# Kernel optimization log

Hardware: AMD Instinct MI355X
Metric: run time of the kernel (lower is better)

Reference implementation:

```python
import jax, jax.numpy as jnp
import numpy as np
from jax import lax

NPOINT, RADIUS, NSAMPLE = 1024, 0.2, 32
EPS = 1e-5

def _fps(xyz, npoint):
    # farthest point sampling, xyz [B,N,3] -> idx [B,npoint]
    B, N, _ = xyz.shape
    def body(carry, _):
        dist, far = carry  # [B,N], [B]
        c = jnp.take_along_axis(xyz, far[:, None, None], axis=1)  # [B,1,3]
        d = jnp.sum((xyz - c) ** 2, -1)
        dist = jnp.minimum(dist, d)
        nxt = jnp.argmax(dist, -1).astype(jnp.int32)
        return (dist, nxt), far
    init = (jnp.full((B, N), 1e10, xyz.dtype), jnp.zeros((B,), jnp.int32))
    _, idx = lax.scan(body, init, None, length=npoint)
    return jnp.transpose(idx)  # [B,npoint]

def _index_points(pts, idx):
    # pts [B,N,C], idx [B,...] int -> [B,...,C]
    return jax.vmap(lambda p, i: p[i])(pts, idx)

def _ball_query(radius, nsample, xyz, new_xyz):
    B, N, _ = xyz.shape
    sqr = (jnp.sum(new_xyz ** 2, -1)[:, :, None] + jnp.sum(xyz ** 2, -1)[:, None, :]
           - 2.0 * jnp.einsum('bsc,bnc->bsn', new_xyz, xyz))  # [B,S,N]
    base = jnp.arange(N, dtype=jnp.int32)[None, None, :]
    idx = jnp.where(sqr > radius ** 2, N, base)
    idx = jnp.sort(idx, -1)[..., :nsample]  # [B,S,K]
    first = idx[..., :1]
    return jnp.where(idx == N, jnp.broadcast_to(first, idx.shape), idx)

def _mlp_bn_relu(x, w, b, g, beta):
    # x [B,C,K,S]; 1x1 conv == channel GEMM; BN uses batch stats (training mode)
    x = jnp.einsum('bcks,oc->boks', x, w) + b[None, :, None, None]
    mu = jnp.mean(x, axis=(0, 2, 3), keepdims=True)
    var = jnp.var(x, axis=(0, 2, 3), keepdims=True)
    x = (x - mu) * lax.rsqrt(var + EPS) * g[None, :, None, None] + beta[None, :, None, None]
    return jax.nn.relu(x)

def setup_inputs() -> dict:
    key = jax.random.key(0)
    ks = jax.random.split(key, 16)
    B, N, D = 16, 4096, 3
    mlp = [64, 64, 128]
    inp = {
        'xyz': jax.random.uniform(ks[0], (B, 3, N), jnp.float32),
        'features': jax.random.normal(ks[1], (B, D, N), jnp.float32),
    }
    last = 3 + D
    for i, c in enumerate(mlp):
        inp[f'w{i}'] = jax.random.normal(ks[2 + 4 * i], (c, last), jnp.float32) * (1.0 / np.sqrt(last))
        inp[f'b{i}'] = jnp.zeros((c,), jnp.float32)
        inp[f'g{i}'] = jnp.ones((c,), jnp.float32)
        inp[f'bt{i}'] = jnp.zeros((c,), jnp.float32)
        last = c
    return inp

def reference(xyz, features, w0, b0, g0, bt0, w1, b1, g1, bt1, w2, b2, g2, bt2):
    xyz_t = jnp.transpose(xyz, (0, 2, 1))        # [B,N,3]
    feat_t = jnp.transpose(features, (0, 2, 1))  # [B,N,D]
    fps_idx = _fps(xyz_t, NPOINT)
    new_xyz = _index_points(xyz_t, fps_idx)      # [B,S,3]
    idx = _ball_query(RADIUS, NSAMPLE, xyz_t, new_xyz)  # [B,S,K]
    grouped_xyz = _index_points(xyz_t, idx) - new_xyz[:, :, None, :]  # [B,S,K,3]
    grouped_feat = _index_points(feat_t, idx)                          # [B,S,K,D]
    x = jnp.concatenate([grouped_xyz, grouped_feat], -1)               # [B,S,K,3+D]
    x = jnp.transpose(x, (0, 3, 2, 1))           # [B,C,K,S]
    for (w, b, g, beta) in ((w0, b0, g0, bt0), (w1, b1, g1, bt1), (w2, b2, g2, bt2)):
        x = _mlp_bn_relu(x, w, b, g, beta)
    new_features = jnp.max(x, axis=2)            # [B,C',S]
    return jnp.transpose(new_xyz, (0, 2, 1)), new_features
```

## Files before the change

kernel.cpp:

```cpp
#include <hip/hip_runtime.h>
#include <hip/hip_bf16.h>
#include <stdint.h>

#define NB 16
#define NPTS 4096
#define NS 1024
#define NK 32
#define NT_COLS (NB*NS*NK)
#define NBUCK 64

typedef __hip_bfloat16 bf16;
typedef __attribute__((ext_vector_type(8))) short short8;
typedef __attribute__((ext_vector_type(4))) float floatx4;
typedef __attribute__((ext_vector_type(2))) float f32x2;

__device__ __forceinline__ unsigned short f2bf_bits(float v) {
  bf16 b = __float2bfloat16(v);
  return *(unsigned short*)&b;
}

template<int CTRL, int RM, int BM>
__device__ __forceinline__ float fmax_dpp(float x) {
  int o = __builtin_amdgcn_update_dpp(__float_as_int(x), __float_as_int(x),
                                      CTRL, RM, BM, false);
  return fmaxf(x, __int_as_float(o));
}
template<int CTRL, int RM>
__device__ __forceinline__ float add_dpp(float x) {
  int o = __builtin_amdgcn_update_dpp(0, __float_as_int(x), CTRL, RM, 0xF, true);
  return __fadd_rn(x, __int_as_float(o));
}
__device__ __forceinline__ float add16_dpp(float x) {
  x = add_dpp<0x111,0xF>(x); x = add_dpp<0x112,0xF>(x);
  x = add_dpp<0x114,0xF>(x); x = add_dpp<0x118,0xF>(x);
  return x;
}
__device__ __forceinline__ float add64_dpp(float x) {
  x = add_dpp<0x111,0xF>(x); x = add_dpp<0x112,0xF>(x);
  x = add_dpp<0x114,0xF>(x); x = add_dpp<0x118,0xF>(x);
  x = add_dpp<0x142,0xA>(x);
  x = add_dpp<0x143,0xC>(x);
  return x;
}

__global__ __launch_bounds__(256) void k_fps(const float* __restrict__ xyz,
                                             float* __restrict__ newxyz,
                                             float* __restrict__ out0,
                                             float* __restrict__ zero_region) {
  const int b = blockIdx.x;
  const int t = threadIdx.x;
  {
    float* zp = zero_region + (size_t)b*2048 + t;
    #pragma unroll
    for (int j = 0; j < 8; ++j) zp[j*256] = 0.f;
  }
  __shared__ float xs[NPTS], ys[NPTS], zs[NPTS];
  __shared__ float selx[NS], sely[NS], selz[NS];
  __shared__ float2 pair[2][4];
  const float* p = xyz + (size_t)b * 3 * NPTS;
  for (int i = t; i < NPTS; i += 256) {
    xs[i] = p[i];
    ys[i] = p[NPTS + i];
    zs[i] = p[2*NPTS + i];
  }
  __syncthreads();
  f32x2 px[8], py[8], pz[8];
  float dist[16];
  const int p0 = t * 16;
  #pragma unroll
  for (int j2 = 0; j2 < 8; ++j2) {
    px[j2] = (f32x2){xs[p0+2*j2], xs[p0+2*j2+1]};
    py[j2] = (f32x2){ys[p0+2*j2], ys[p0+2*j2+1]};
    pz[j2] = (f32x2){zs[p0+2*j2], zs[p0+2*j2+1]};
    dist[2*j2] = 1e10f; dist[2*j2+1] = 1e10f;
  }
  const int lane = t & 63, wv = t >> 6;
  int cur = 0;
  for (int i = 0; i < NS; ++i) {
    float cx = xs[cur], cy = ys[cur], cz = zs[cur];
    if (t == 0) { selx[i] = cx; sely[i] = cy; selz[i] = cz; }
    if (i == NS-1) break;
    const f32x2 ncx = (f32x2){-cx, -cx};
    const f32x2 ncy = (f32x2){-cy, -cy};
    const f32x2 ncz = (f32x2){-cz, -cz};
    float bv = -1.0f; int bi = p0;
    #pragma unroll
    for (int j2 = 0; j2 < 8; ++j2) {
      f32x2 d;
      {
        #pragma clang fp contract(off)
        f32x2 dx = px[j2] + ncx;
        f32x2 dy = py[j2] + ncy;
        f32x2 dz = pz[j2] + ncz;
        d = dx*dx + dy*dy + dz*dz;
      }
      float nd0 = fminf(dist[2*j2],   d.x);
      float nd1 = fminf(dist[2*j2+1], d.y);
      dist[2*j2] = nd0; dist[2*j2+1] = nd1;
      if (nd0 > bv) { bv = nd0; bi = p0 + 2*j2; }
      if (nd1 > bv) { bv = nd1; bi = p0 + 2*j2 + 1; }
    }
    float x = bv;
    x = fmax_dpp<0x111,0xF,0xF>(x);
    x = fmax_dpp<0x112,0xF,0xF>(x);
    x = fmax_dpp<0x114,0xF,0xF>(x);
    x = fmax_dpp<0x118,0xF,0xF>(x);
    x = fmax_dpp<0x142,0xA,0xF>(x);
    x = fmax_dpp<0x143,0xC,0xF>(x);
    float M = __int_as_float(__builtin_amdgcn_readlane(__float_as_int(x), 63));
    unsigned long long mk = __ballot(bv == M);
    int sl  = (int)__builtin_ctzll(mk);
    int wbi = __builtin_amdgcn_readlane(bi, sl);
    if ((t & 63) == 0) pair[i & 1][wv] = make_float2(M, __int_as_float(wbi));
    __syncthreads();
    const float4* pb = (const float4*)&pair[i & 1][0];
    float4 q01 = pb[0], q23 = pb[1];
    float bestv = q01.x; int besti = __float_as_int(q01.y);
    if (q01.z > bestv) { bestv = q01.z; besti = __float_as_int(q01.w); }
    if (q23.x > bestv) { bestv = q23.x; besti = __float_as_int(q23.y); }
    if (q23.z > bestv) { bestv = q23.z; besti = __float_as_int(q23.w); }
    cur = besti;
  }
  __syncthreads();
  for (int i = t; i < NS; i += 256) {
    float vx = selx[i], vy = sely[i], vz = selz[i];
    size_t q = (size_t)b*3*NS + i;
    out0[q] = vx; out0[q + NS] = vy; out0[q + 2*NS] = vz;
    size_t o = (size_t)(b*NS + i)*3;
    newxyz[o] = vx; newxyz[o+1] = vy; newxyz[o+2] = vz;
  }
}

__global__ __launch_bounds__(256) void k_ballq(const float* __restrict__ xyz,
                                               const float* __restrict__ newxyz,
                                               int* __restrict__ idx) {
  __shared__ float xs[NPTS], ys[NPTS], zs[NPTS];
  const int b  = blockIdx.x >> 8;
  const int s  = (blockIdx.x & 255) * 4 + (threadIdx.x >> 6);
  const int lane = threadIdx.x & 63;
  const float* p = xyz + (size_t)b * 3 * NPTS;
  for (int i = threadIdx.x; i < NPTS; i += 256) {
    xs[i] = p[i];
    ys[i] = p[NPTS + i];
    zs[i] = p[2*NPTS + i];
  }
  __syncthreads();
  const size_t nq = (size_t)(b*NS + s)*3;
  const float nx = newxyz[nq], ny = newxyz[nq+1], nz = newxyz[nq+2];
  const float sn = __fadd_rn(__fadd_rn(__fmul_rn(nx,nx), __fmul_rn(ny,ny)), __fmul_rn(nz,nz));
  const float R2 = (float)(0.2*0.2);
  int* out = idx + (size_t)(b*NS + s) * NK;
  int cnt = 0, first = 0;
  for (int c0 = 0; c0 < NPTS; c0 += 64) {
    int n = c0 + lane;
    float x = xs[n], y = ys[n], z = zs[n];
    float sx = __fadd_rn(__fadd_rn(__fmul_rn(x,x), __fmul_rn(y,y)), __fmul_rn(z,z));
    float dt = __fadd_rn(__fadd_rn(__fmul_rn(nx,x), __fmul_rn(ny,y)), __fmul_rn(nz,z));
    float sqr = __fsub_rn(__fadd_rn(sn, sx), __fmul_rn(2.0f, dt));
    bool inr = (sqr <= R2);
    unsigned long long m = __ballot(inr);
    if (m != 0ull) {
      if (cnt == 0) first = c0 + (int)__builtin_ctzll(m);
      int rank = __popcll(m & ((1ull << lane) - 1ull));
      int pos = cnt + rank;
      if (inr && pos < NK) out[pos] = n;
      cnt += __popcll(m);
      if (cnt >= NK) break;
    }
  }
  int tot = cnt < NK ? cnt : NK;
  if (lane >= tot && lane < NK) out[lane] = first;
}

__global__ __launch_bounds__(256) void k_moments(const float* __restrict__ xyz,
                                                 const float* __restrict__ feat,
                                                 const float* __restrict__ newxyz,
                                                 const int* __restrict__ idx,
                                                 float* __restrict__ accum) {
  const int t = threadIdx.x;
  float S[6] = {0,0,0,0,0,0};
  float Mm[21];
  #pragma unroll
  for (int k = 0; k < 21; ++k) Mm[k] = 0.f;
  for (int it = 0; it < 8; ++it) {
    const int col = blockIdx.x*2048 + it*256 + t;
    const int bs = col >> 5;
    const int b  = bs >> 10;
    const int n  = idx[col];
    const float* xb = xyz  + (size_t)b*3*NPTS;
    const float* fb = feat + (size_t)b*3*NPTS;
    float u[6];
    u[0] = __fsub_rn(xb[n],        newxyz[(size_t)bs*3]);
    u[1] = __fsub_rn(xb[NPTS+n],   newxyz[(size_t)bs*3+1]);
    u[2] = __fsub_rn(xb[2*NPTS+n], newxyz[(size_t)bs*3+2]);
    u[3] = fb[n];
    u[4] = fb[NPTS+n];
    u[5] = fb[2*NPTS+n];
    int k = 0;
    #pragma unroll
    for (int i = 0; i < 6; ++i) {
      S[i] += u[i];
      #pragma unroll
      for (int j = i; j < 6; ++j) { Mm[k] = fmaf(u[i], u[j], Mm[k]); ++k; }
    }
  }
  const int lane = t & 63;
  float* dst = accum + (size_t)(blockIdx.x & (NBUCK-1))*32;
  #pragma unroll
  for (int i = 0; i < 6; ++i) {
    float s = add64_dpp(S[i]);
    if (lane == 63) atomicAdd(&dst[i], s);
  }
  #pragma unroll
  for (int k = 0; k < 21; ++k) {
    float m = add64_dpp(Mm[k]);
    if (lane == 63) atomicAdd(&dst[6+k], m);
  }
}

__global__ void k_finalize1(const float* __restrict__ accum,
                            const float* __restrict__ w0, const float* __restrict__ b0,
                            const float* __restrict__ g, const float* __restrict__ beta,
                            float* __restrict__ scsh) {
  __shared__ float Sm[27];
  const int t = threadIdx.x;
  if (t < 27) {
    float s = 0.f;
    for (int bkt = 0; bkt < NBUCK; ++bkt) s += accum[(size_t)bkt*32 + t];
    Sm[t] = s;
  }
  __syncthreads();
  if (t < 64) {
    const float* w = w0 + t*6;
    const float b = b0[t];
    float ws = 0.f;
    #pragma unroll
    for (int i = 0; i < 6; ++i) ws = fmaf(w[i], Sm[i], ws);
    float quad = 0.f;
    int k = 6;
    #pragma unroll
    for (int i = 0; i < 6; ++i) {
      #pragma unroll
      for (int j = i; j < 6; ++j) {
        float c = w[i]*w[j];
        if (j > i) c *= 2.f;
        quad = fmaf(c, Sm[k], quad);
        ++k;
      }
    }
    const float n = (float)NT_COLS;
    float mean = (ws + n*b) / n;
    float ex2  = (quad + 2.f*b*ws + n*b*b) / n;
    float var  = ex2 - mean*mean;
    if (var < 0.f) var = 0.f;
    float rs = rsqrtf(var + 1e-5f);
    float sc = g[t] * rs;
    scsh[t]    = sc;
    scsh[64+t] = beta[t] - mean * sc;
  }
}

__global__ void k_finalize(const float* __restrict__ accum,
                           const float* __restrict__ g, const float* __restrict__ beta,
                           float* __restrict__ scsh, int C) {
  int o = threadIdx.x;
  if (o < C) {
    float s = 0.f, ss = 0.f;
    for (int bkt = 0; bkt < NBUCK; ++bkt) {
      s  += accum[(size_t)bkt*(2*C) + o];
      ss += accum[(size_t)bkt*(2*C) + C + o];
    }
    const float n = (float)NT_COLS;
    float mu  = s / n;
    float var = ss / n - mu*mu;
    if (var < 0.f) var = 0.f;
    float rs = rsqrtf(var + 1e-5f);
    float sc = g[o] * rs;
    scsh[o]   = sc;
    scsh[C+o] = beta[o] - mu * sc;
  }
}

#define XT_STRIDE 72

__global__ __launch_bounds__(256) void k_layer2_mfma(
    const float* __restrict__ xyz,
    const float* __restrict__ feat,
    const float* __restrict__ newxyz,
    const int*   __restrict__ idx,
    const float* __restrict__ w0g,
    const float* __restrict__ b0g,
    const float* __restrict__ w1,
    const float* __restrict__ b1,
    const float* __restrict__ scsh,
    float*       __restrict__ accum,
    bf16*        __restrict__ x2) {
  __shared__ short xT[256*XT_STRIDE];
  __shared__ float w0s[64*6];
  __shared__ float b0s[64];
  __shared__ float sc_s[64], sh_s[64], bias_s[64];
  const int t = threadIdx.x;
  const int col0 = blockIdx.x * 256;
  for (int i = t; i < 64*6; i += 256) w0s[i] = w0g[i];
  if (t < 64) {
    b0s[t] = b0g[t];
    sc_s[t] = scsh[t]; sh_s[t] = scsh[64+t];
    bias_s[t] = b1[t];
  }
  __syncthreads();
  {
    const int col = col0 + t;
    const int bs = col >> 5;
    const int b  = bs >> 10;
    const int n  = idx[col];
    const float* xb = xyz  + (size_t)b*3*NPTS;
    const float* fb = feat + (size_t)b*3*NPTS;
    float u[6];
    u[0] = __fsub_rn(xb[n],        newxyz[(size_t)bs*3]);
    u[1] = __fsub_rn(xb[NPTS+n],   newxyz[(size_t)bs*3+1]);
    u[2] = __fsub_rn(xb[2*NPTS+n], newxyz[(size_t)bs*3+2]);
    u[3] = fb[n];
    u[4] = fb[NPTS+n];
    u[5] = fb[2*NPTS+n];
    #pragma unroll
    for (int c0 = 0; c0 < 64; c0 += 8) {
      short8 pk;
      #pragma unroll
      for (int j = 0; j < 8; ++j) {
        const int o = c0 + j;
        float v = b0s[o];
        #pragma unroll
        for (int c = 0; c < 6; ++c) v = fmaf(u[c], w0s[o*6+c], v);
        v = fmaxf(fmaf(v, sc_s[o], sh_s[o]), 0.f);
        pk[j] = (short)f2bf_bits(v);
      }
      *((short8*)&xT[t*XT_STRIDE + c0]) = pk;
    }
  }
  __syncthreads();
  const int lane = t & 63, wv = t >> 6;
  const int qd = lane >> 4, ln = lane & 15;
  short8 A[4][2];
  #pragma unroll
  for (int rt = 0; rt < 4; ++rt) {
    #pragma unroll
    for (int kh = 0; kh < 2; ++kh) {
      const float* wp = w1 + (size_t)(rt*16 + ln)*64 + kh*32 + qd*8;
      float4 f0 = *(const float4*)wp;
      float4 f1 = *(const float4*)(wp + 4);
      short8 a;
      a[0]=(short)f2bf_bits(f0.x); a[1]=(short)f2bf_bits(f0.y);
      a[2]=(short)f2bf_bits(f0.z); a[3]=(short)f2bf_bits(f0.w);
      a[4]=(short)f2bf_bits(f1.x); a[5]=(short)f2bf_bits(f1.y);
      a[6]=(short)f2bf_bits(f1.z); a[7]=(short)f2bf_bits(f1.w);
      A[rt][kh] = a;
    }
  }
  floatx4 acc[4][4];
  #pragma unroll
  for (int rt = 0; rt < 4; ++rt)
    #pragma unroll
    for (int ct = 0; ct < 4; ++ct)
      acc[rt][ct] = (floatx4)0.f;
  #pragma unroll
  for (int ct = 0; ct < 4; ++ct) {
    const int coll = wv*64 + ct*16 + ln;
    short8 B0 = *((const short8*)&xT[coll*XT_STRIDE + qd*8]);
    short8 B1 = *((const short8*)&xT[coll*XT_STRIDE + 32 + qd*8]);
    #pragma unroll
    for (int rt = 0; rt < 4; ++rt) {
      acc[rt][ct] = __builtin_amdgcn_mfma_f32_16x16x32_bf16(A[rt][0], B0, acc[rt][ct], 0,0,0);
      acc[rt][ct] = __builtin_amdgcn_mfma_f32_16x16x32_bf16(A[rt][1], B1, acc[rt][ct], 0,0,0);
    }
  }
  float* dst = accum + (size_t)(blockIdx.x & (NBUCK-1))*128;
  #pragma unroll
  for (int rt = 0; rt < 4; ++rt) {
    float s[4]  = {0.f,0.f,0.f,0.f};
    float sq[4] = {0.f,0.f,0.f,0.f};
    #pragma unroll
    for (int ct = 0; ct < 4; ++ct) {
      const int col = col0 + wv*64 + ct*16 + ln;
      #pragma unroll
      for (int r = 0; r < 4; ++r) {
        const int o = rt*16 + qd*4 + r;
        float v = acc[rt][ct][r] + bias_s[o];
        x2[(size_t)o*NT_COLS + col] = __float2bfloat16(v);
        s[r] += v; sq[r] = fmaf(v, v, sq[r]);
      }
    }
    #pragma unroll
    for (int r = 0; r < 4; ++r) {
      float a = add16_dpp(s[r]);
      float q = add16_dpp(sq[r]);
      if (ln == 15) {
        const int o = rt*16 + qd*4 + r;
        atomicAdd(&dst[o], a);
        atomicAdd(&dst[64 + o], q);
      }
    }
  }
}

__global__ __launch_bounds__(256) void k_layer3_mfma(
    const bf16*  __restrict__ xin,
    const float* __restrict__ wN,
    const float* __restrict__ bN,
    const float* __restrict__ scsh,
    float*       __restrict__ accum,
    float*       __restrict__ mx) {
  constexpr int CO = 128, RT = CO/16;
  __shared__ short xT[256*XT_STRIDE];
  __shared__ float sc_s[64], sh_s[64], bias_s[CO];
  const int t = threadIdx.x;
  const int col0 = blockIdx.x * 256;
  if (t < 64) { sc_s[t] = scsh[t]; sh_s[t] = scsh[64+t]; }
  if (t < CO) bias_s[t] = bN[t];
  __syncthreads();
  {
    const int col = col0 + t;
    #pragma unroll
    for (int c0 = 0; c0 < 64; c0 += 8) {
      short8 pk;
      #pragma unroll
      for (int j = 0; j < 8; ++j) {
        float v = __bfloat162float(xin[(size_t)(c0+j)*NT_COLS + col]);
        v = fmaxf(fmaf(v, sc_s[c0+j], sh_s[c0+j]), 0.f);
        pk[j] = (short)f2bf_bits(v);
      }
      *((short8*)&xT[t*XT_STRIDE + c0]) = pk;
    }
  }
  __syncthreads();
  const int lane = t & 63, wv = t >> 6;
  const int qd = lane >> 4, ln = lane & 15;
  short8 A[RT][2];
  #pragma unroll
  for (int rt = 0; rt < RT; ++rt) {
    #pragma unroll
    for (int kh = 0; kh < 2; ++kh) {
      const float* wp = wN + (size_t)(rt*16 + ln)*64 + kh*32 + qd*8;
      float4 f0 = *(const float4*)wp;
      float4 f1 = *(const float4*)(wp + 4);
      short8 a;
      a[0]=(short)f2bf_bits(f0.x); a[1]=(short)f2bf_bits(f0.y);
      a[2]=(short)f2bf_bits(f0.z); a[3]=(short)f2bf_bits(f0.w);
      a[4]=(short)f2bf_bits(f1.x); a[5]=(short)f2bf_bits(f1.y);
      a[6]=(short)f2bf_bits(f1.z); a[7]=(short)f2bf_bits(f1.w);
      A[rt][kh] = a;
    }
  }
  floatx4 acc[RT][4];
  #pragma unroll
  for (int rt = 0; rt < RT; ++rt)
    #pragma unroll
    for (int ct = 0; ct < 4; ++ct)
      acc[rt][ct] = (floatx4)0.f;
  #pragma unroll
  for (int ct = 0; ct < 4; ++ct) {
    const int coll = wv*64 + ct*16 + ln;
    short8 B0 = *((const short8*)&xT[coll*XT_STRIDE + qd*8]);
    short8 B1 = *((const short8*)&xT[coll*XT_STRIDE + 32 + qd*8]);
    #pragma unroll
    for (int rt = 0; rt < RT; ++rt) {
      acc[rt][ct] = __builtin_amdgcn_mfma_f32_16x16x32_bf16(A[rt][0], B0, acc[rt][ct], 0,0,0);
      acc[rt][ct] = __builtin_amdgcn_mfma_f32_16x16x32_bf16(A[rt][1], B1, acc[rt][ct], 0,0,0);
    }
  }
  float* dst = accum + (size_t)(blockIdx.x & (NBUCK-1))*(2*CO);
  const int bs0 = (col0 + wv*64) >> 5;
  #pragma unroll
  for (int rt = 0; rt < RT; ++rt) {
    float s[4]  = {0.f,0.f,0.f,0.f};
    float sq[4] = {0.f,0.f,0.f,0.f};
    float mxv[2][4];
    #pragma unroll
    for (int h = 0; h < 2; ++h)
      #pragma unroll
      for (int r = 0; r < 4; ++r) mxv[h][r] = -3.402823466e38f;
    #pragma unroll
    for (int ct = 0; ct < 4; ++ct) {
      #pragma unroll
      for (int r = 0; r < 4; ++r) {
        const int o = rt*16 + qd*4 + r;
        float v = acc[rt][ct][r] + bias_s[o];
        mxv[ct>>1][r] = fmaxf(mxv[ct>>1][r], v);
        s[r] += v; sq[r] = fmaf(v, v, sq[r]);
      }
    }
    #pragma unroll
    for (int h = 0; h < 2; ++h) {
      #pragma unroll
      for (int r = 0; r < 4; ++r) {
        float m = mxv[h][r];
        m = fmax_dpp<0x111,0xF,0xF>(m);
        m = fmax_dpp<0x112,0xF,0xF>(m);
        m = fmax_dpp<0x114,0xF,0xF>(m);
        m = fmax_dpp<0x118,0xF,0xF>(m);
        if (ln == 15) {
          const int o = rt*16 + qd*4 + r;
          mx[(size_t)o*(NT_COLS/NK) + bs0 + h] = m;
        }
      }
    }
    #pragma unroll
    for (int r = 0; r < 4; ++r) {
      float a = add16_dpp(s[r]);
      float q = add16_dpp(sq[r]);
      if (ln == 15) {
        const int o = rt*16 + qd*4 + r;
        atomicAdd(&dst[o], a);
        atomicAdd(&dst[CO + o], q);
      }
    }
  }
}

__global__ __launch_bounds__(256) void k_bnmax(const float* __restrict__ mx,
                                               const float* __restrict__ scsh,
                                               float* __restrict__ out1) {
  const int blk = blockIdx.x;
  const int o = blk & 127;
  const int b = blk >> 7;
  const float sc = scsh[o], sh = scsh[128+o];
  const int s = threadIdx.x * 4;
  float4 v = *(const float4*)(mx + (size_t)o*(NT_COLS/NK) + b*NS + s);
  float4 r;
  r.x = fmaxf(fmaf(v.x, sc, sh), 0.f);
  r.y = fmaxf(fmaf(v.y, sc, sh), 0.f);
  r.z = fmaxf(fmaf(v.z, sc, sh), 0.f);
  r.w = fmaxf(fmaf(v.w, sc, sh), 0.f);
  *(float4*)(out1 + (size_t)(b*128 + o)*NS + s) = r;
}

extern "C" void kernel_launch(void* const* d_in, const int* in_sizes, int n_in,
                              void* d_out, int out_size, void* d_ws, size_t ws_size,
                              hipStream_t stream) {
  const float* xyz  = (const float*)d_in[0];
  const float* feat = (const float*)d_in[1];
  const float* w0 = (const float*)d_in[2];
  const float* b0 = (const float*)d_in[3];
  const float* g0 = (const float*)d_in[4];
  const float* bt0= (const float*)d_in[5];
  const float* w1 = (const float*)d_in[6];
  const float* b1 = (const float*)d_in[7];
  const float* g1 = (const float*)d_in[8];
  const float* bt1= (const float*)d_in[9];
  const float* w2 = (const float*)d_in[10];
  const float* b2 = (const float*)d_in[11];
  const float* g2 = (const float*)d_in[12];
  const float* bt2= (const float*)d_in[13];

  float* out0 = (float*)d_out;
  float* out1 = out0 + (size_t)NB*3*NS;

  char* ws = (char*)d_ws;
  float* accum  = (float*)(ws + 0);
  float* acc_l1 = accum;
  float* acc_l2 = accum + 8192;
  float* acc_l3 = accum + 16384;
  float* scsh   = (float*)(ws + 131072);
  float* newxyz = (float*)(ws + 133120);
  int*   bidx   = (int*)  (ws + 329728);
  bf16*  x2     = (bf16*) (ws + 2426880);
  float* mx3    = (float*)(ws + 136644608);

  k_fps  <<<NB, 256, 0, stream>>>(xyz, newxyz, out0, accum);
  k_ballq<<<NB*256, 256, 0, stream>>>(xyz, newxyz, bidx);

  k_moments  <<<256, 256, 0, stream>>>(xyz, feat, newxyz, bidx, acc_l1);
  k_finalize1<<<1,    64, 0, stream>>>(acc_l1, w0, b0, g0, bt0, scsh + 0);

  k_layer2_mfma<<<NT_COLS/256, 256, 0, stream>>>(xyz, feat, newxyz, bidx,
                                                 w0, b0, w1, b1, scsh + 0,
                                                 acc_l2, x2);
  k_finalize<<<1, 256, 0, stream>>>(acc_l2, g1, bt1, scsh + 128, 64);

  k_layer3_mfma<<<NT_COLS/256, 256, 0, stream>>>(x2, w2, b2, scsh + 128,
                                                 acc_l3, mx3);
  k_finalize<<<1, 256, 0, stream>>>(acc_l3, g2, bt2, scsh + 256, 128);

  k_bnmax <<<NB*128, 256, 0, stream>>>(mx3, scsh + 256, out1);
}
```

Measured before the change: 816.8 us.

## Carry winner coordinates in FPS reduction and pack four batches per block

```diff
diff --git a/kernel.cpp b/kernel.cpp
--- a/kernel.cpp
+++ b/kernel.cpp
@@ -43,47 +43,56 @@
   return x;
 }
 
-__global__ __launch_bounds__(256) void k_fps(const float* __restrict__ xyz,
-                                             float* __restrict__ newxyz,
-                                             float* __restrict__ out0,
-                                             float* __restrict__ zero_region) {
-  const int b = blockIdx.x;
+__global__ __launch_bounds__(1024) void k_fps(const float* __restrict__ xyz,
+                                              float* __restrict__ newxyz,
+                                              float* __restrict__ out0,
+                                              float* __restrict__ zero_region) {
   const int t = threadIdx.x;
   {
-    float* zp = zero_region + (size_t)b*2048 + t;
-    #pragma unroll
-    for (int j = 0; j < 8; ++j) zp[j*256] = 0.f;
-  }
-  __shared__ float xs[NPTS], ys[NPTS], zs[NPTS];
-  __shared__ float selx[NS], sely[NS], selz[NS];
-  __shared__ float2 pair[2][4];
+    float* zp = zero_region + (size_t)blockIdx.x*8192 + t;
+    #pragma unroll
+    for (int j = 0; j < 8; ++j) zp[j*1024] = 0.f;
+  }
+  const int half = t >> 8;
+  const int tl   = t & 255;
+  const int b    = blockIdx.x*4 + half;
+  const int lane = t & 63;
+  const int wv4  = tl >> 6;
+  __shared__ __align__(16) float4 pair[2][4][4];
   const float* p = xyz + (size_t)b * 3 * NPTS;
-  for (int i = t; i < NPTS; i += 256) {
-    xs[i] = p[i];
-    ys[i] = p[NPTS + i];
-    zs[i] = p[2*NPTS + i];
-  }
-  __syncthreads();
+
   f32x2 px[8], py[8], pz[8];
   float dist[16];
-  const int p0 = t * 16;
-  #pragma unroll
-  for (int j2 = 0; j2 < 8; ++j2) {
-    px[j2] = (f32x2){xs[p0+2*j2], xs[p0+2*j2+1]};
-    py[j2] = (f32x2){ys[p0+2*j2], ys[p0+2*j2+1]};
-    pz[j2] = (f32x2){zs[p0+2*j2], zs[p0+2*j2+1]};
-    dist[2*j2] = 1e10f; dist[2*j2+1] = 1e10f;
-  }
-  const int lane = t & 63, wv = t >> 6;
-  int cur = 0;
+  const int p0 = tl * 16;
+  {
+    const float4* xp = (const float4*)(p + p0);
+    const float4* yp = (const float4*)(p + NPTS + p0);
+    const float4* zp4 = (const float4*)(p + 2*NPTS + p0);
+    #pragma unroll
+    for (int q = 0; q < 4; ++q) {
+      float4 ax = xp[q], ay = yp[q], az = zp4[q];
+      px[2*q]   = (f32x2){ax.x, ax.y};  px[2*q+1] = (f32x2){ax.z, ax.w};
+      py[2*q]   = (f32x2){ay.x, ay.y};  py[2*q+1] = (f32x2){ay.z, ay.w};
+      pz[2*q]   = (f32x2){az.x, az.y};  pz[2*q+1] = (f32x2){az.z, az.w};
+    }
+    #pragma unroll
+    for (int j = 0; j < 16; ++j) dist[j] = 1e10f;
+  }
+  float cx = p[0], cy = p[NPTS], cz = p[2*NPTS];
+
   for (int i = 0; i < NS; ++i) {
-    float cx = xs[cur], cy = ys[cur], cz = zs[cur];
-    if (t == 0) { selx[i] = cx; sely[i] = cy; selz[i] = cz; }
+    if (tl == 0) {
+      size_t q = (size_t)b*3*NS + i;
+      out0[q] = cx; out0[q + NS] = cy; out0[q + 2*NS] = cz;
+      size_t o = (size_t)(b*NS + i)*3;
+      newxyz[o] = cx; newxyz[o+1] = cy; newxyz[o+2] = cz;
+    }
     if (i == NS-1) break;
     const f32x2 ncx = (f32x2){-cx, -cx};
     const f32x2 ncy = (f32x2){-cy, -cy};
     const f32x2 ncz = (f32x2){-cz, -cz};
-    float bv = -1.0f; int bi = p0;
+    float bv = -1.0f;
+    float bx = px[0].x, by = py[0].x, bz = pz[0].x;
     #pragma unroll
     for (int j2 = 0; j2 < 8; ++j2) {
       f32x2 d;
@@ -97,8 +106,8 @@
       float nd0 = fminf(dist[2*j2],   d.x);
       float nd1 = fminf(dist[2*j2+1], d.y);
       dist[2*j2] = nd0; dist[2*j2+1] = nd1;
-      if (nd0 > bv) { bv = nd0; bi = p0 + 2*j2; }
-      if (nd1 > bv) { bv = nd1; bi = p0 + 2*j2 + 1; }
+      if (nd0 > bv) { bv = nd0; bx = px[j2].x; by = py[j2].x; bz = pz[j2].x; }
+      if (nd1 > bv) { bv = nd1; bx = px[j2].y; by = py[j2].y; bz = pz[j2].y; }
     }
     float x = bv;
     x = fmax_dpp<0x111,0xF,0xF>(x);
@@ -109,25 +118,19 @@
     x = fmax_dpp<0x143,0xC,0xF>(x);
     float M = __int_as_float(__builtin_amdgcn_readlane(__float_as_int(x), 63));
     unsigned long long mk = __ballot(bv == M);
-    int sl  = (int)__builtin_ctzll(mk);
-    int wbi = __builtin_amdgcn_readlane(bi, sl);
-    if ((t & 63) == 0) pair[i & 1][wv] = make_float2(M, __int_as_float(wbi));
+    int sl = (int)__builtin_ctzll(mk);
+    float wx = __int_as_float(__builtin_amdgcn_readlane(__float_as_int(bx), sl));
+    float wy = __int_as_float(__builtin_amdgcn_readlane(__float_as_int(by), sl));
+    float wz = __int_as_float(__builtin_amdgcn_readlane(__float_as_int(bz), sl));
+    if (lane == 0) pair[i & 1][half][wv4] = make_float4(M, wx, wy, wz);
     __syncthreads();
-    const float4* pb = (const float4*)&pair[i & 1][0];
-    float4 q01 = pb[0], q23 = pb[1];
-    float bestv = q01.x; int besti = __float_as_int(q01.y);
-    if (q01.z > bestv) { bestv = q01.z; besti = __float_as_int(q01.w); }
-    if (q23.x > bestv) { bestv = q23.x; besti = __float_as_int(q23.y); }
-    if (q23.z > bestv) { bestv = q23.z; besti = __float_as_int(q23.w); }
-    cur = besti;
-  }
-  __syncthreads();
-  for (int i = t; i < NS; i += 256) {
-    float vx = selx[i], vy = sely[i], vz = selz[i];
-    size_t q = (size_t)b*3*NS + i;
-    out0[q] = vx; out0[q + NS] = vy; out0[q + 2*NS] = vz;
-    size_t o = (size_t)(b*NS + i)*3;
-    newxyz[o] = vx; newxyz[o+1] = vy; newxyz[o+2] = vz;
+    const float4* pb = &pair[i & 1][half][0];
+    float4 q0 = pb[0], q1 = pb[1], q2 = pb[2], q3 = pb[3];
+    float4 best = q0;
+    if (q1.x > best.x) best = q1;
+    if (q2.x > best.x) best = q2;
+    if (q3.x > best.x) best = q3;
+    cx = best.y; cy = best.z; cz = best.w;
   }
 }
 
@@ -565,7 +568,7 @@
   bf16*  x2     = (bf16*) (ws + 2426880);
   float* mx3    = (float*)(ws + 136644608);
 
-  k_fps  <<<NB, 256, 0, stream>>>(xyz, newxyz, out0, accum);
+  k_fps  <<<NB/4, 1024, 0, stream>>>(xyz, newxyz, out0, accum);
   k_ballq<<<NB*256, 256, 0, stream>>>(xyz, newxyz, bidx);
 
   k_moments  <<<256, 256, 0, stream>>>(xyz, feat, newxyz, bidx, acc_l1);
```

Measured after the change: 2.044 ms. 2.5x slower.
